# Performance work log

Measured on AMD Instinct MI355X. Metric: run time of the kernel, lower is better.

Reference implementation:

```python
import jax, jax.numpy as jnp
import numpy as np

B, D, H, G, WR = 8192, 1024, 1024, 2, 64
URANKS = [64, 64]


def setup_inputs() -> dict:
    key = jax.random.key(0)
    ks = jax.random.split(key, 12)
    s = 0.1
    return {
        "x": jax.random.normal(ks[0], (B, D), jnp.float32),
        "h": jax.random.normal(ks[1], (B, H), jnp.float32),
        "c": jax.random.normal(ks[2], (B, H), jnp.float32),
        "dia_x": s * jax.random.normal(ks[3], (1, D), jnp.float32),
        "dia_h": s * jax.random.normal(ks[4], (1, H), jnp.float32),
        "Ux": s * jax.random.normal(ks[5], (D, WR), jnp.float32),
        "Vx": s * jax.random.normal(ks[6], (4 * H, WR), jnp.float32),
        "Uh_0": s * jax.random.normal(ks[7], (G, H // G, URANKS[0]), jnp.float32),
        "Vh_0": s * jax.random.normal(ks[8], (G, URANKS[0], 4 * (H // G)), jnp.float32),
        "Uh_1": s * jax.random.normal(ks[9], (G, H // G, URANKS[1]), jnp.float32),
        "Vh_1": s * jax.random.normal(ks[10], (G, URANKS[1], 4 * (H // G)), jnp.float32),
        "bias_x": jnp.ones((1, 4 * H), jnp.float32),
        "bias_h": jnp.ones((1, 4 * H), jnp.float32),
    }


def reference(x, h, c, dia_x, dia_h, Ux, Vx, Uh_0, Vh_0, Uh_1, Vh_1, bias_x, bias_h):
    Bn, Dn = x.shape
    Hn = h.shape[1]
    g = Uh_0.shape[0]
    Hg = Hn // g
    r0 = Uh_0.shape[2]

    # diagonal (vector-multiplication) paths, x-part zero-padded to hidden width
    vm_x = jnp.pad(dia_x * x, ((0, 0), (0, Hn - Dn)))          # [B, H]
    vm_h = dia_h * h                                           # [B, H]

    # low-rank input projection
    lowered_x = (x @ Ux) @ Vx.T                                # [B, 4H]

    # refined diagonal corrections subtracted from the low-rank outputs
    Vx4 = Vx.reshape(4, Hn, -1)[:, :Dn, :]                     # [4, D, wR]
    coef_x = jnp.sum(Ux[None, :, :] * Vx4, axis=-1)            # [4, D]
    vm_refined_x = jnp.pad(x[:, None, :] * coef_x[None], ((0, 0), (0, 0), (0, Hn - Dn))).reshape(Bn, 4 * Hn)

    Uh0f = Uh_0.reshape(Hn, r0)                                # [H, r0]
    Vh0f = jnp.transpose(Vh_0, (0, 2, 1)).reshape(4 * Hn, r0).reshape(4, Hn, r0)
    coef_h = jnp.sum(Uh0f[None, :, :] * Vh0f, axis=-1)         # [4, H]
    vm_refined_h = (h[:, None, :] * coef_h[None]).reshape(Bn, 4 * Hn)

    gx = lowered_x - vm_refined_x + bias_x
    xi, xf, xo, xn = jnp.split(gx, 4, axis=1)

    # grouped low-rank recurrent projection with cyclic group permutation
    hv = h.reshape(Bn, g, Hg)
    Uhs = [Uh_0, Uh_1]
    Vhs = [Vh_0, Vh_1]
    g_h = jnp.zeros((Bn, 4 * Hn), x.dtype)
    for i in range(g):
        idx = np.roll(np.arange(g), -i)                        # static permutation
        hp = hv[:, idx, :]                                     # [B, g, H/g]
        t = jnp.einsum('bgn,gnr->bgr', hp, Uhs[i])             # [B, g, r_i]
        t = jnp.einsum('bgr,grm->bgm', t, Vhs[i])              # [B, g, 4H/g]
        g_h = g_h + t.reshape(Bn, 4 * Hn)

    gh = g_h - vm_refined_h + bias_h
    hf, hi, hn, ho = jnp.split(gh, 4, axis=1)                  # note gate order differs from x

    base = vm_x + vm_h
    inputgate = jax.nn.sigmoid(xi + hi + base)
    forgetgate = jax.nn.sigmoid(xf + hf + base)
    outputgate = jax.nn.sigmoid(xo + ho + base)
    newgate = jnp.tanh(xn + hn + base)

    c_next = forgetgate * c + inputgate * newgate
    h_next = outputgate * jnp.tanh(c_next)
    return (h_next, c_next)
```

## Files before the change

kernel.cpp:

```cpp
#include <hip/hip_runtime.h>


typedef _Float16 half8 __attribute__((ext_vector_type(8)));
typedef _Float16 half4v __attribute__((ext_vector_type(4)));
typedef float f32x4 __attribute__((ext_vector_type(4)));

#define WS_TA    0
#define WS_TB    3145728
#define WS_U1F   6291456
#define WS_UH1F  6422528
#define WS_W2    6684672
#define WS_CX    8257536
#define WS_CH    8273920
#define WS_BB    8290304

__global__ __launch_bounds__(256) void prep_kernel(
    const float* __restrict__ Ux, const float* __restrict__ Vx,
    const float* __restrict__ Uh0, const float* __restrict__ Vh0,
    const float* __restrict__ Uh1, const float* __restrict__ Vh1,
    const float* __restrict__ dia_x, const float* __restrict__ dia_h,
    const float* __restrict__ bias_x, const float* __restrict__ bias_h,
    _Float16* __restrict__ U1f, _Float16* __restrict__ Uh1f,
    _Float16* __restrict__ W2f, float* __restrict__ cx,
    float* __restrict__ ch, float* __restrict__ bb)
{
    int e = blockIdx.x * 256 + threadIdx.x;
    if (e < 8192) {
        int lane = e & 63, ks = (e >> 6) & 31, ct = e >> 11;
        int l15 = lane & 15, quad = lane >> 4;
        half8 v8;
        #pragma unroll
        for (int jj = 0; jj < 8; ++jj) {
            int k = ks * 32 + quad * 8 + jj;
            v8[jj] = (_Float16)Ux[k * 64 + ct * 16 + l15];
        }
        *(half8*)&U1f[(size_t)e * 8] = v8;
    } else if (e < 24576) {
        int t = e - 8192;
        int lane = t & 63, ks = (t >> 6) & 15, ct = (t >> 10) & 3, j = t >> 12;
        int l15 = lane & 15, quad = lane >> 4;
        const float* src = (j & 1) ? Uh1 : Uh0;
        int g = j >> 1;
        half8 v8;
        #pragma unroll
        for (int jj = 0; jj < 8; ++jj) {
            int k = ks * 32 + quad * 8 + jj;
            v8[jj] = (_Float16)src[(g * 512 + k) * 64 + ct * 16 + l15];
        }
        *(half8*)&Uh1f[(size_t)t * 8] = v8;
    } else if (e < 122880) {
        int t = e - 24576;
        int lane = t & 63;
        int ksq  = (t >> 6) % 6;
        int ct   = (t / 384) & 63;
        int g01  = (t / 24576) & 1;
        int s    = t / 49152;
        int l15 = lane & 15, quad = lane >> 4;
        int k = ct * 16 + l15;
        int jx = s * 2 + g01;
        int m = (g01 == 0) ? (1024 + k) : k;
        half8 v8;
        #pragma unroll
        for (int jj = 0; jj < 8; ++jj) {
            int kk = ksq * 32 + quad * 8 + jj;
            int r = kk & 63, sect = kk >> 6;
            float val;
            if (sect == 0)      val = Vx[(jx * 1024 + k) * 64 + r];
            else if (sect == 1) val = Vh0[(s * 64 + r) * 2048 + m];
            else                val = Vh1[(s * 64 + r) * 2048 + m];
            v8[jj] = (_Float16)val;
        }
        *(half8*)&W2f[(size_t)t * 8] = v8;
    } else if (e < 126976) {
        int t = e - 122880; int q = t >> 10; int k = t & 1023;
        int jh = q ^ 1;
        int fh = jh * 1024 + k; int g = fh >> 11; int m = fh & 2047;
        float sx = 0.f, sh = 0.f;
        for (int r = 0; r < 64; ++r) {
            sx += Ux[k * 64 + r] * Vx[(q * 1024 + k) * 64 + r];
            sh += Uh0[k * 64 + r] * Vh0[(g * 64 + r) * 2048 + m];
        }
        cx[t] = dia_x[k] - sx;
        ch[t] = dia_h[k] - sh;
        bb[t] = bias_x[q * 1024 + k] + bias_h[jh * 1024 + k];
    }
}

__global__ __launch_bounds__(256) void s1_kernel(
    const float* __restrict__ x, const float* __restrict__ h,
    const _Float16* __restrict__ U1f, const _Float16* __restrict__ Uh1f,
    _Float16* __restrict__ Ta, _Float16* __restrict__ Tb)
{
    __shared__ __align__(16) _Float16 Ash[16][520];

    const int job = blockIdx.y;
    const int b0 = blockIdx.x * 16;
    const int tid = threadIdx.x;
    const int w = tid >> 6, l = tid & 63, l15 = l & 15, quad = l >> 4;

    f32x4 acc0 = {}, acc1 = {};
    const int nkc = (job == 0) ? 2 : 1;
    const float* src = (job == 0) ? x : h;

    for (int kc = 0; kc < nkc; ++kc) {
        const int koff = (job == 2) ? 512 : kc * 512;
        #pragma unroll
        for (int ii = 0; ii < 8; ++ii) {
            int idx = tid + ii * 256;
            int row = idx >> 7, c4 = idx & 127;
            float4 f = *(const float4*)&src[(size_t)(b0 + row) * 1024 + koff + c4 * 4];
            half4v p;
            p[0] = (_Float16)f.x; p[1] = (_Float16)f.y;
            p[2] = (_Float16)f.z; p[3] = (_Float16)f.w;
            *(half4v*)&Ash[row][c4 * 4] = p;
        }
        __syncthreads();
        if (job == 0) {
            const _Float16* bp = U1f + ((size_t)(w * 32 + kc * 16) * 64 + l) * 8;
            #pragma unroll
            for (int ks = 0; ks < 16; ++ks) {
                half8 a = *(const half8*)&Ash[l15][ks * 32 + quad * 8];
                half8 b = *(const half8*)(bp + (size_t)ks * 512);
                acc0 = __builtin_amdgcn_mfma_f32_16x16x32_f16(a, b, acc0, 0, 0, 0);
            }
        } else {
            const int j0 = (job == 1) ? 0 : 1;
            const int j1 = (job == 1) ? 3 : 2;
            const _Float16* bp0 = Uh1f + ((size_t)((j0 * 4 + w) * 16) * 64 + l) * 8;
            const _Float16* bp1 = Uh1f + ((size_t)((j1 * 4 + w) * 16) * 64 + l) * 8;
            #pragma unroll
            for (int ks = 0; ks < 16; ++ks) {
                half8 a = *(const half8*)&Ash[l15][ks * 32 + quad * 8];
                half8 b0 = *(const half8*)(bp0 + (size_t)ks * 512);
                acc0 = __builtin_amdgcn_mfma_f32_16x16x32_f16(a, b0, acc0, 0, 0, 0);
                half8 b1 = *(const half8*)(bp1 + (size_t)ks * 512);
                acc1 = __builtin_amdgcn_mfma_f32_16x16x32_f16(a, b1, acc1, 0, 0, 0);
            }
        }
        __syncthreads();
    }
    if (job == 0) {
        int col = w * 16 + l15;
        #pragma unroll
        for (int r = 0; r < 4; ++r) {
            int row = b0 + quad * 4 + r;
            _Float16 v = (_Float16)acc0[r];
            Ta[(size_t)row * 192 + col] = v;
            Tb[(size_t)row * 192 + col] = v;
        }
    } else {
        int colA = ((job == 1) ? 64 : 128) + w * 16 + l15;
        int colB = ((job == 1) ? 128 : 64) + w * 16 + l15;
        #pragma unroll
        for (int r = 0; r < 4; ++r) {
            int row = b0 + quad * 4 + r;
            Ta[(size_t)row * 192 + colA] = (_Float16)acc0[r];
            Tb[(size_t)row * 192 + colB] = (_Float16)acc1[r];
        }
    }
}

__global__ __launch_bounds__(256, 4) void s2_kernel(
    const _Float16* __restrict__ Ta, const _Float16* __restrict__ Tb,
    const _Float16* __restrict__ W2f,
    const float* __restrict__ cx, const float* __restrict__ ch,
    const float* __restrict__ bb,
    const float* __restrict__ x, const float* __restrict__ h,
    const float* __restrict__ c, float* __restrict__ out)
{
    __shared__ __align__(16) _Float16 TaSh[32][200];
    __shared__ __align__(16) _Float16 TbSh[32][200];

    const int b0 = blockIdx.x * 32;
    const int by = blockIdx.y;
    const int tid = threadIdx.x;
    const int w = tid >> 6, l = tid & 63, l15 = l & 15, quad = l >> 4;

    #pragma unroll
    for (int ii = 0; ii < 6; ++ii) {
        int idx = tid + ii * 256;
        int arr = idx >= 768;
        int i2 = idx - (arr ? 768 : 0);
        int row = i2 / 24, c8 = i2 % 24;
        const _Float16* src = arr ? Tb : Ta;
        _Float16* dst = arr ? &TbSh[row][c8 * 8] : &TaSh[row][c8 * 8];
        *(half8*)dst = *(const half8*)&src[(size_t)(b0 + row) * 192 + c8 * 8];
    }
    __syncthreads();

    const size_t laneoff = (size_t)l * 8;

    #pragma unroll
    for (int kr = 0; kr < 2; ++kr) {
        const int ctg = by * 8 + kr * 4 + w;
        const int k = ctg * 16 + l15;
        f32x4 acc[4][2] = {};
        const _Float16* bpi = W2f + (size_t)((0 * 64 + ctg) * 6) * 512 + laneoff;
        const _Float16* bpf = W2f + (size_t)((1 * 64 + ctg) * 6) * 512 + laneoff;
        const _Float16* bpo = W2f + (size_t)((2 * 64 + ctg) * 6) * 512 + laneoff;
        const _Float16* bpn = W2f + (size_t)((3 * 64 + ctg) * 6) * 512 + laneoff;
        #pragma unroll
        for (int ks = 0; ks < 6; ++ks) {
            half8 bi = *(const half8*)(bpi + (size_t)ks * 512);
            half8 bf = *(const half8*)(bpf + (size_t)ks * 512);
            half8 bo = *(const half8*)(bpo + (size_t)ks * 512);
            half8 bn = *(const half8*)(bpn + (size_t)ks * 512);
            #pragma unroll
            for (int rt = 0; rt < 2; ++rt) {
                half8 aA = *(const half8*)&TaSh[rt * 16 + l15][ks * 32 + quad * 8];
                half8 aB = *(const half8*)&TbSh[rt * 16 + l15][ks * 32 + quad * 8];
                acc[0][rt] = __builtin_amdgcn_mfma_f32_16x16x32_f16(aA, bi, acc[0][rt], 0, 0, 0);
                acc[1][rt] = __builtin_amdgcn_mfma_f32_16x16x32_f16(aA, bf, acc[1][rt], 0, 0, 0);
                acc[2][rt] = __builtin_amdgcn_mfma_f32_16x16x32_f16(aB, bo, acc[2][rt], 0, 0, 0);
                acc[3][rt] = __builtin_amdgcn_mfma_f32_16x16x32_f16(aB, bn, acc[3][rt], 0, 0, 0);
            }
        }
        float cxi = cx[k], cxf = cx[1024 + k], cxo = cx[2048 + k], cxn = cx[3072 + k];
        float chi = ch[k], chf = ch[1024 + k], cho = ch[2048 + k], chn = ch[3072 + k];
        float bbi = bb[k], bbf = bb[1024 + k], bbo = bb[2048 + k], bbn = bb[3072 + k];
        #pragma unroll
        for (int rt = 0; rt < 2; ++rt) {
            #pragma unroll
            for (int r = 0; r < 4; ++r) {
                int row = b0 + rt * 16 + quad * 4 + r;
                size_t off = (size_t)row * 1024 + k;
                float xv = x[off], hv = h[off], cv = c[off];
                float pi = acc[0][rt][r] + xv * cxi + hv * chi + bbi;
                float pf = acc[1][rt][r] + xv * cxf + hv * chf + bbf;
                float po = acc[2][rt][r] + xv * cxo + hv * cho + bbo;
                float pn = acc[3][rt][r] + xv * cxn + hv * chn + bbn;
                float ig = __builtin_amdgcn_rcpf(1.f + __expf(-pi));
                float fg = __builtin_amdgcn_rcpf(1.f + __expf(-pf));
                float og = __builtin_amdgcn_rcpf(1.f + __expf(-po));
                float ng = 1.f - 2.f * __builtin_amdgcn_rcpf(__expf(2.f * pn) + 1.f);
                float cn = fg * cv + ig * ng;
                float tc = 1.f - 2.f * __builtin_amdgcn_rcpf(__expf(2.f * cn) + 1.f);
                out[off] = og * tc;
                out[(size_t)8388608 + off] = cn;
            }
        }
    }
}

extern "C" void kernel_launch(void* const* d_in, const int* in_sizes, int n_in,
                              void* d_out, int out_size, void* d_ws, size_t ws_size,
                              hipStream_t stream)
{
    const float* x      = (const float*)d_in[0];
    const float* h      = (const float*)d_in[1];
    const float* c      = (const float*)d_in[2];
    const float* dia_x  = (const float*)d_in[3];
    const float* dia_h  = (const float*)d_in[4];
    const float* Ux     = (const float*)d_in[5];
    const float* Vx     = (const float*)d_in[6];
    const float* Uh0    = (const float*)d_in[7];
    const float* Vh0    = (const float*)d_in[8];
    const float* Uh1    = (const float*)d_in[9];
    const float* Vh1    = (const float*)d_in[10];
    const float* bias_x = (const float*)d_in[11];
    const float* bias_h = (const float*)d_in[12];
    float* out = (float*)d_out;

    char* ws = (char*)d_ws;
    _Float16* TaW  = (_Float16*)(ws + WS_TA);
    _Float16* TbW  = (_Float16*)(ws + WS_TB);
    _Float16* U1f  = (_Float16*)(ws + WS_U1F);
    _Float16* Uh1f = (_Float16*)(ws + WS_UH1F);
    _Float16* W2f  = (_Float16*)(ws + WS_W2);
    float* cx = (float*)(ws + WS_CX);
    float* ch = (float*)(ws + WS_CH);
    float* bb = (float*)(ws + WS_BB);

    prep_kernel<<<496, 256, 0, stream>>>(Ux, Vx, Uh0, Vh0, Uh1, Vh1,
                                         dia_x, dia_h, bias_x, bias_h,
                                         U1f, Uh1f, W2f, cx, ch, bb);
    s1_kernel<<<dim3(512, 3), 256, 0, stream>>>(x, h, U1f, Uh1f, TaW, TbW);
    s2_kernel<<<dim3(256, 8), 256, 0, stream>>>(TaW, TbW, W2f, cx, ch, bb,
                                                x, h, c, out);
}
```

Before: 244.6 us.

## Merge Ta/Tb intermediates, wave-parallelize coef reduction, prefetch x/h/c in s2

Replaces the two duplicated 192-column fp16 intermediates with a single 320-column buffer, so the shared x-projection columns are written once and s2 loads one smaller tile into LDS. The prep kernel's serial 64-term dot products for the diagonal corrections become one wave per output, reduced with xor shuffles, which adds far more threads to prep. In s2, the x/h/c loads for the epilogue are issued before the MFMA loop to hide their latency, and the kr loop is no longer unrolled. The cost is more registers held live across the MFMA loop and a different LDS indexing pattern for the second operand.

```diff
diff --git a/kernel.cpp b/kernel.cpp
--- a/kernel.cpp
+++ b/kernel.cpp
@@ -5,14 +5,13 @@
 typedef _Float16 half4v __attribute__((ext_vector_type(4)));
 typedef float f32x4 __attribute__((ext_vector_type(4)));
 
-#define WS_TA    0
-#define WS_TB    3145728
-#define WS_U1F   6291456
-#define WS_UH1F  6422528
-#define WS_W2    6684672
-#define WS_CX    8257536
-#define WS_CH    8273920
-#define WS_BB    8290304
+#define WS_TM    0
+#define WS_U1F   5242880
+#define WS_UH1F  5373952
+#define WS_W2    5636096
+#define WS_CX    7208960
+#define WS_CH    7225344
+#define WS_BB    7241728
 
 __global__ __launch_bounds__(256) void prep_kernel(
     const float* __restrict__ Ux, const float* __restrict__ Vx,
@@ -71,25 +70,32 @@
             v8[jj] = (_Float16)val;
         }
         *(half8*)&W2f[(size_t)t * 8] = v8;
-    } else if (e < 126976) {
-        int t = e - 122880; int q = t >> 10; int k = t & 1023;
+    } else if (e < 385024) {
+        int t = e - 122880;
+        int r = t & 63;
+        int wid = t >> 6;
+        int q = wid >> 10, k = wid & 1023;
         int jh = q ^ 1;
         int fh = jh * 1024 + k; int g = fh >> 11; int m = fh & 2047;
-        float sx = 0.f, sh = 0.f;
-        for (int r = 0; r < 64; ++r) {
-            sx += Ux[k * 64 + r] * Vx[(q * 1024 + k) * 64 + r];
-            sh += Uh0[k * 64 + r] * Vh0[(g * 64 + r) * 2048 + m];
-        }
-        cx[t] = dia_x[k] - sx;
-        ch[t] = dia_h[k] - sh;
-        bb[t] = bias_x[q * 1024 + k] + bias_h[jh * 1024 + k];
+        float sx = Ux[k * 64 + r] * Vx[(q * 1024 + k) * 64 + r];
+        float sh = Uh0[k * 64 + r] * Vh0[(g * 64 + r) * 2048 + m];
+        #pragma unroll
+        for (int msk = 1; msk < 64; msk <<= 1) {
+            sx += __shfl_xor(sx, msk, 64);
+            sh += __shfl_xor(sh, msk, 64);
+        }
+        if (r == 0) {
+            cx[wid] = dia_x[k] - sx;
+            ch[wid] = dia_h[k] - sh;
+            bb[wid] = bias_x[q * 1024 + k] + bias_h[jh * 1024 + k];
+        }
     }
 }
 
 __global__ __launch_bounds__(256) void s1_kernel(
     const float* __restrict__ x, const float* __restrict__ h,
     const _Float16* __restrict__ U1f, const _Float16* __restrict__ Uh1f,
-    _Float16* __restrict__ Ta, _Float16* __restrict__ Tb)
+    _Float16* __restrict__ Tm)
 {
     __shared__ __align__(16) _Float16 Ash[16][520];
 
@@ -144,32 +150,28 @@
         #pragma unroll
         for (int r = 0; r < 4; ++r) {
             int row = b0 + quad * 4 + r;
-            _Float16 v = (_Float16)acc0[r];
-            Ta[(size_t)row * 192 + col] = v;
-            Tb[(size_t)row * 192 + col] = v;
+            Tm[(size_t)row * 320 + col] = (_Float16)acc0[r];
         }
     } else {
         int colA = ((job == 1) ? 64 : 128) + w * 16 + l15;
-        int colB = ((job == 1) ? 128 : 64) + w * 16 + l15;
+        int colB = ((job == 1) ? 256 : 192) + w * 16 + l15;
         #pragma unroll
         for (int r = 0; r < 4; ++r) {
             int row = b0 + quad * 4 + r;
-            Ta[(size_t)row * 192 + colA] = (_Float16)acc0[r];
-            Tb[(size_t)row * 192 + colB] = (_Float16)acc1[r];
+            Tm[(size_t)row * 320 + colA] = (_Float16)acc0[r];
+            Tm[(size_t)row * 320 + colB] = (_Float16)acc1[r];
         }
     }
 }
 
 __global__ __launch_bounds__(256, 4) void s2_kernel(
-    const _Float16* __restrict__ Ta, const _Float16* __restrict__ Tb,
-    const _Float16* __restrict__ W2f,
+    const _Float16* __restrict__ Tm, const _Float16* __restrict__ W2f,
     const float* __restrict__ cx, const float* __restrict__ ch,
     const float* __restrict__ bb,
     const float* __restrict__ x, const float* __restrict__ h,
     const float* __restrict__ c, float* __restrict__ out)
 {
-    __shared__ __align__(16) _Float16 TaSh[32][200];
-    __shared__ __align__(16) _Float16 TbSh[32][200];
+    __shared__ __align__(16) _Float16 TmSh[32][328];
 
     const int b0 = blockIdx.x * 32;
     const int by = blockIdx.y;
@@ -177,23 +179,29 @@
     const int w = tid >> 6, l = tid & 63, l15 = l & 15, quad = l >> 4;
 
     #pragma unroll
-    for (int ii = 0; ii < 6; ++ii) {
-        int idx = tid + ii * 256;
-        int arr = idx >= 768;
-        int i2 = idx - (arr ? 768 : 0);
-        int row = i2 / 24, c8 = i2 % 24;
-        const _Float16* src = arr ? Tb : Ta;
-        _Float16* dst = arr ? &TbSh[row][c8 * 8] : &TaSh[row][c8 * 8];
-        *(half8*)dst = *(const half8*)&src[(size_t)(b0 + row) * 192 + c8 * 8];
+    for (int ii = 0; ii < 5; ++ii) {
+        int i2 = tid + ii * 256;
+        int row = i2 / 40, c8 = i2 % 40;
+        *(half8*)&TmSh[row][c8 * 8] = *(const half8*)&Tm[(size_t)(b0 + row) * 320 + c8 * 8];
     }
     __syncthreads();
 
     const size_t laneoff = (size_t)l * 8;
 
-    #pragma unroll
+    #pragma unroll 1
     for (int kr = 0; kr < 2; ++kr) {
         const int ctg = by * 8 + kr * 4 + w;
         const int k = ctg * 16 + l15;
+        float xv[2][4], hv[2][4], cv[2][4];
+        #pragma unroll
+        for (int rt = 0; rt < 2; ++rt)
+            #pragma unroll
+            for (int r = 0; r < 4; ++r) {
+                size_t off = (size_t)(b0 + rt * 16 + quad * 4 + r) * 1024 + k;
+                xv[rt][r] = x[off];
+                hv[rt][r] = h[off];
+                cv[rt][r] = c[off];
+            }
         f32x4 acc[4][2] = {};
         const _Float16* bpi = W2f + (size_t)((0 * 64 + ctg) * 6) * 512 + laneoff;
         const _Float16* bpf = W2f + (size_t)((1 * 64 + ctg) * 6) * 512 + laneoff;
@@ -205,10 +213,12 @@
             half8 bf = *(const half8*)(bpf + (size_t)ks * 512);
             half8 bo = *(const half8*)(bpo + (size_t)ks * 512);
             half8 bn = *(const half8*)(bpn + (size_t)ks * 512);
+            const int aoff = ks * 32 + quad * 8;
+            const int boff = ((ks < 2) ? ks * 32 : 128 + ks * 32) + quad * 8;
             #pragma unroll
             for (int rt = 0; rt < 2; ++rt) {
-                half8 aA = *(const half8*)&TaSh[rt * 16 + l15][ks * 32 + quad * 8];
-                half8 aB = *(const half8*)&TbSh[rt * 16 + l15][ks * 32 + quad * 8];
+                half8 aA = *(const half8*)&TmSh[rt * 16 + l15][aoff];
+                half8 aB = *(const half8*)&TmSh[rt * 16 + l15][boff];
                 acc[0][rt] = __builtin_amdgcn_mfma_f32_16x16x32_f16(aA, bi, acc[0][rt], 0, 0, 0);
                 acc[1][rt] = __builtin_amdgcn_mfma_f32_16x16x32_f16(aA, bf, acc[1][rt], 0, 0, 0);
                 acc[2][rt] = __builtin_amdgcn_mfma_f32_16x16x32_f16(aB, bo, acc[2][rt], 0, 0, 0);
@@ -224,16 +234,15 @@
             for (int r = 0; r < 4; ++r) {
                 int row = b0 + rt * 16 + quad * 4 + r;
                 size_t off = (size_t)row * 1024 + k;
-                float xv = x[off], hv = h[off], cv = c[off];
-                float pi = acc[0][rt][r] + xv * cxi + hv * chi + bbi;
-                float pf = acc[1][rt][r] + xv * cxf + hv * chf + bbf;
-                float po = acc[2][rt][r] + xv * cxo + hv * cho + bbo;
-                float pn = acc[3][rt][r] + xv * cxn + hv * chn + bbn;
+                float pi = acc[0][rt][r] + xv[rt][r] * cxi + hv[rt][r] * chi + bbi;
+                float pf = acc[1][rt][r] + xv[rt][r] * cxf + hv[rt][r] * chf + bbf;
+                float po = acc[2][rt][r] + xv[rt][r] * cxo + hv[rt][r] * cho + bbo;
+                float pn = acc[3][rt][r] + xv[rt][r] * cxn + hv[rt][r] * chn + bbn;
                 float ig = __builtin_amdgcn_rcpf(1.f + __expf(-pi));
                 float fg = __builtin_amdgcn_rcpf(1.f + __expf(-pf));
                 float og = __builtin_amdgcn_rcpf(1.f + __expf(-po));
                 float ng = 1.f - 2.f * __builtin_amdgcn_rcpf(__expf(2.f * pn) + 1.f);
-                float cn = fg * cv + ig * ng;
+                float cn = fg * cv[rt][r] + ig * ng;
                 float tc = 1.f - 2.f * __builtin_amdgcn_rcpf(__expf(2.f * cn) + 1.f);
                 out[off] = og * tc;
                 out[(size_t)8388608 + off] = cn;
@@ -262,8 +271,7 @@
     float* out = (float*)d_out;
 
     char* ws = (char*)d_ws;
-    _Float16* TaW  = (_Float16*)(ws + WS_TA);
-    _Float16* TbW  = (_Float16*)(ws + WS_TB);
+    _Float16* TmW  = (_Float16*)(ws + WS_TM);
     _Float16* U1f  = (_Float16*)(ws + WS_U1F);
     _Float16* Uh1f = (_Float16*)(ws + WS_UH1F);
     _Float16* W2f  = (_Float16*)(ws + WS_W2);
@@ -271,10 +279,10 @@
     float* ch = (float*)(ws + WS_CH);
     float* bb = (float*)(ws + WS_BB);
 
-    prep_kernel<<<496, 256, 0, stream>>>(Ux, Vx, Uh0, Vh0, Uh1, Vh1,
-                                         dia_x, dia_h, bias_x, bias_h,
-                                         U1f, Uh1f, W2f, cx, ch, bb);
-    s1_kernel<<<dim3(512, 3), 256, 0, stream>>>(x, h, U1f, Uh1f, TaW, TbW);
-    s2_kernel<<<dim3(256, 8), 256, 0, stream>>>(TaW, TbW, W2f, cx, ch, bb,
+    prep_kernel<<<1504, 256, 0, stream>>>(Ux, Vx, Uh0, Vh0, Uh1, Vh1,
+                                          dia_x, dia_h, bias_x, bias_h,
+                                          U1f, Uh1f, W2f, cx, ch, bb);
+    s1_kernel<<<dim3(512, 3), 256, 0, stream>>>(x, h, U1f, Uh1f, TmW);
+    s2_kernel<<<dim3(256, 8), 256, 0, stream>>>(TmW, W2f, cx, ch, bb,
                                                 x, h, c, out);
 }
```

New measurement: 307.1 us. 1.26x slower.
